# Optimization experiments

Hardware: AMD Instinct MI355X
Metric: run time of the kernel (lower is better)

## Reference

```python
import jax, jax.numpy as jnp
import numpy as np

N, E = 50000, 800000
IN_DIM, H0, H1, OUT_DIM = 64, 64, 64, 8
NUM_RELS, NUM_BASES = 16, 8


def setup_inputs() -> dict:
    key = jax.random.key(0)
    ks = jax.random.split(key, 20)
    features = jax.random.normal(ks[0], (N, IN_DIM), dtype=jnp.float32)
    etypes = jax.random.randint(ks[1], (E,), 0, NUM_RELS)
    src = jax.random.randint(ks[2], (E,), 0, N)
    dst = jax.random.randint(ks[3], (E,), 0, N)
    # degree normalization 1/in_degree(dst), as DGL stores in g.edata['norm']
    deg = jax.ops.segment_sum(jnp.ones((E,), jnp.float32), dst, num_segments=N)
    norm = (1.0 / jnp.maximum(deg, 1.0))[dst][:, None]  # [E,1]

    def glorot(k, shape):
        fan_in, fan_out = shape[-2], shape[-1]
        lim = jnp.sqrt(6.0 / (fan_in + fan_out)).astype(jnp.float32)
        return jax.random.uniform(k, shape, jnp.float32, -lim, lim)

    dims = [(IN_DIM, H0), (H0, H1), (H1, OUT_DIM)]
    inp = {"features": features, "norm": norm}
    for i, (di, do) in enumerate(dims):
        inp[f"basis{i}"] = glorot(ks[4 + 4 * i], (NUM_BASES, di, do))
        inp[f"comp{i}"] = glorot(ks[5 + 4 * i], (NUM_RELS, NUM_BASES))
        inp[f"loop{i}"] = glorot(ks[6 + 4 * i], (di, do))
        inp[f"bias{i}"] = jnp.zeros((do,), jnp.float32)
    inp["etypes"] = etypes
    inp["src"] = src
    inp["dst"] = dst
    return inp


def rel_graph_conv(h, basis, comp, loop_w, bias, etypes, src, dst, norm, act):
    # basis-decomposed relation weights: [R, din, dout]
    W = jnp.einsum('rb,bio->rio', comp, basis)
    # transform every node under every relation: [N, R, dout]
    h_trans = jnp.einsum('ni,rio->nro', h, W)
    # per-edge gather of (src node, edge relation), degree-normalized
    msg = h_trans[src, etypes] * norm  # [E, dout]
    agg = jax.ops.segment_sum(msg, dst, num_segments=h.shape[0])  # [N, dout]
    out = agg + h @ loop_w + bias  # self-loop + bias (DGL defaults)
    return act(out)


def reference(features, norm, basis0, comp0, loop0, bias0, basis1, comp1, loop1,
              bias1, basis2, comp2, loop2, bias2, etypes, src, dst):
    lrelu = lambda x: jax.nn.leaky_relu(x, negative_slope=0.01)
    h = rel_graph_conv(features, basis0, comp0, loop0, bias0, etypes, src, dst, norm, lrelu)
    h = rel_graph_conv(h, basis1, comp1, loop1, bias1, etypes, src, dst, norm, lrelu)
    h = rel_graph_conv(h, basis2, comp2, loop2, bias2, etypes, src, dst, norm, jax.nn.relu)
    return h
```

## Files before the change

### kernel.cpp

```cpp
#include <hip/hip_runtime.h>

#define NN 50000
#define NE 800000
#define CAP 64
#define KC 72
#define CSTR 16

typedef __bf16 bf16x8 __attribute__((ext_vector_type(8)));
typedef float f32x4 __attribute__((ext_vector_type(4)));
typedef float f32x2 __attribute__((ext_vector_type(2)));
typedef unsigned short ushort;
typedef unsigned int uint;

__device__ inline ushort f2bf(float x) {
  uint u = __builtin_bit_cast(uint, x);
  u += 0x7FFF + ((u >> 16) & 1);
  return (ushort)(u >> 16);
}
__device__ inline float bf2f(ushort u) {
  return __builtin_bit_cast(float, (uint)u << 16);
}


__device__ inline void wprep_body(const float* __restrict__ basis,
                                  const float* __restrict__ loopw,
                                  ushort* __restrict__ W2, int DOUT, int NCOLS,
                                  int idx) {
  int total = KC * NCOLS * 8;
  if (idx >= total) return;
  int j = idx & 7;
  int n = (idx >> 3) % NCOLS;
  int kc = idx / (8 * NCOLS);
  int k = kc * 8 + j;
  float v = 0.f;
  if (n < DOUT) v = (k < 512) ? basis[k * DOUT + n] : loopw[(k - 512) * DOUT + n];
  W2[((size_t)kc * NCOLS + n) * 8 + j] = f2bf(v);
}

__global__ __launch_bounds__(256) void build_kernel(
    const int* __restrict__ dstv, const int* __restrict__ srcv,
    const int* __restrict__ etv, int* __restrict__ cursor, int* __restrict__ pk,
    const float* __restrict__ f, ushort* __restrict__ fb,
    const float* __restrict__ b0, const float* __restrict__ l0, ushort* __restrict__ W0,
    const float* __restrict__ b1, const float* __restrict__ l1, ushort* __restrict__ W1,
    const float* __restrict__ b2, const float* __restrict__ l2, ushort* __restrict__ W2,
    const float* __restrict__ c0, const float* __restrict__ c1,
    const float* __restrict__ c2, float* __restrict__ cp) {
  int blk = blockIdx.x;
  int tid = threadIdx.x;
  if (blk < 3125) {
    int i = blk * 256 + tid;
    int d = dstv[i];
    int p = atomicAdd(&cursor[(size_t)d * CSTR], 1);
    if (p < CAP) pk[d * CAP + p] = (etv[i] << 16) | srcv[i];
  } else if (blk < 6250) {
    int i = (blk - 3125) * 256 + tid;
    float4 v = ((const float4*)f)[i];
    ushort4 u;
    u.x = f2bf(v.x); u.y = f2bf(v.y); u.z = f2bf(v.z); u.w = f2bf(v.w);
    ((ushort4*)fb)[i] = u;
  } else if (blk < 6394) {
    wprep_body(b0, l0, W0, 64, 64, (blk - 6250) * 256 + tid);
  } else if (blk < 6538) {
    wprep_body(b1, l1, W1, 64, 64, (blk - 6394) * 256 + tid);
  } else if (blk < 6574) {
    wprep_body(b2, l2, W2, 8, 16, (blk - 6538) * 256 + tid);
  } else {
    int idx = (blk - 6574) * 256 + tid;
    if (idx < 408) {
      int l = idx / 136, k = idx % 136;
      const float* src = (l == 0) ? c0 : ((l == 1) ? c1 : c2);
      cp[idx] = (k < 128) ? src[k] : 0.f;
    }
  }
}


template <int DOUT, int NCOLS, bool OBF>
__global__ __launch_bounds__(1024, 8) void layer_kernel(
    const ushort* __restrict__ hb,
    const float* __restrict__ cpad,
    const int* __restrict__ degv,
    const int* __restrict__ pk,
    const ushort* __restrict__ W2,
    const float* __restrict__ bias,
    void* __restrict__ outp,
    float slope)
{
  __shared__ ushort X[KC][16][8];
  int tid = threadIdx.x;
  int wave = tid >> 6;
  int lane = tid & 63;
  int dbase = blockIdx.x * 16;
  int d = __builtin_amdgcn_readfirstlane(dbase + wave);

  int deg = degv[(size_t)d * CSTR];
  int dw = deg > CAP ? CAP : deg;
  const int4* p4 = (const int4*)(pk + (size_t)d * CAP);

  f32x2 acc2[4] = {{0.f, 0.f}, {0.f, 0.f}, {0.f, 0.f}, {0.f, 0.f}};
  for (int base = 0; base < dw; base += 8) {
    int qg = base >> 3;
    int4 e0 = p4[qg * 2];
    int4 e1 = p4[qg * 2 + 1];
    int pe[8] = {e0.x, e0.y, e0.z, e0.w, e1.x, e1.y, e1.z, e1.w};
    float hv[8];
    int ps[8];
#pragma unroll
    for (int i = 0; i < 8; ++i) {
      int pr = __builtin_amdgcn_readfirstlane(pe[i]);
      ps[i] = (base + i < dw) ? pr : (16 << 16);
      hv[i] = bf2f(hb[(size_t)(ps[i] & 0xFFFF) * 64 + lane]);
    }
#pragma unroll
    for (int i = 0; i < 8; ++i) {
      const f32x2* c2 = (const f32x2*)(cpad + (ps[i] >> 16) * 8);
      f32x2 h2 = {hv[i], hv[i]};
#pragma unroll
      for (int j = 0; j < 4; ++j)
        acc2[j] = __builtin_elementwise_fma(c2[j], h2, acc2[j]);
    }
  }

  float inv = 1.0f / (float)(deg > 1 ? deg : 1);
  int jj = lane & 7;
  int csub = lane >> 3;
#pragma unroll
  for (int b = 0; b < 8; ++b) {
    float v = ((b & 1) ? acc2[b >> 1].y : acc2[b >> 1].x) * inv;
    X[b * 8 + csub][wave ^ csub][jj] = f2bf(v);
  }
  X[64 + csub][wave ^ csub][jj] = hb[(size_t)d * 64 + lane];
  __syncthreads();

  if (wave < (DOUT == 64 ? 4 : 1)) {
    int q = lane >> 4;
    int r = lane & 15;
    f32x4 accd = {0.f, 0.f, 0.f, 0.f};
#pragma unroll
    for (int ks = 0; ks < 18; ++ks) {
      int kc = ks * 4 + q;
      bf16x8 bfrag = *(const bf16x8*)&X[kc][r ^ (kc & 7)][0];
      bf16x8 afrag = *(const bf16x8*)(W2 + ((size_t)kc * NCOLS + wave * 16 + r) * 8);
      accd = __builtin_amdgcn_mfma_f32_16x16x32_bf16(afrag, bfrag, accd, 0, 0, 0);
    }
    int m = dbase + r;
    int nb = wave * 16 + q * 4;
    if (nb < DOUT) {
      float4 bv = *(const float4*)(bias + nb);
      float v0 = accd[0] + bv.x;
      float v1 = accd[1] + bv.y;
      float v2 = accd[2] + bv.z;
      float v3 = accd[3] + bv.w;
      v0 = v0 > 0.f ? v0 : slope * v0;
      v1 = v1 > 0.f ? v1 : slope * v1;
      v2 = v2 > 0.f ? v2 : slope * v2;
      v3 = v3 > 0.f ? v3 : slope * v3;
      if (OBF) {
        ushort4 u;
        u.x = f2bf(v0); u.y = f2bf(v1); u.z = f2bf(v2); u.w = f2bf(v3);
        *(ushort4*)((ushort*)outp + (size_t)m * DOUT + nb) = u;
      } else {
        *(float4*)((float*)outp + (size_t)m * DOUT + nb) = float4{v0, v1, v2, v3};
      }
    }
  }
}


extern "C" void kernel_launch(void* const* d_in, const int* in_sizes, int n_in,
                              void* d_out, int out_size, void* d_ws, size_t ws_size,
                              hipStream_t stream) {
  const float* features = (const float*)d_in[0];
  const float* basis0   = (const float*)d_in[2];
  const float* comp0    = (const float*)d_in[3];
  const float* loop0    = (const float*)d_in[4];
  const float* bias0    = (const float*)d_in[5];
  const float* basis1   = (const float*)d_in[6];
  const float* comp1    = (const float*)d_in[7];
  const float* loop1    = (const float*)d_in[8];
  const float* bias1    = (const float*)d_in[9];
  const float* basis2   = (const float*)d_in[10];
  const float* comp2    = (const float*)d_in[11];
  const float* loop2    = (const float*)d_in[12];
  const float* bias2    = (const float*)d_in[13];
  const int* etypes     = (const int*)d_in[14];
  const int* srcv       = (const int*)d_in[15];
  const int* dstv       = (const int*)d_in[16];

  char* ws = (char*)d_ws;
  size_t off = 0;
  auto alloc = [&](size_t bytes) {
    void* p = ws + off;
    off += (bytes + 255) & ~(size_t)255;
    return p;
  };
  int* cnt      = (int*)alloc((size_t)NN * CSTR * sizeof(int));
  int* pk       = (int*)alloc((size_t)NN * CAP * sizeof(int));
  ushort* W2_0  = (ushort*)alloc((size_t)KC * 64 * 8 * sizeof(ushort));
  ushort* W2_1  = (ushort*)alloc((size_t)KC * 64 * 8 * sizeof(ushort));
  ushort* W2_2  = (ushort*)alloc((size_t)KC * 16 * 8 * sizeof(ushort));
  float* cpad   = (float*)alloc(3 * 136 * sizeof(float));
  ushort* fbf   = (ushort*)alloc((size_t)NN * 64 * sizeof(ushort));
  ushort* hA    = (ushort*)alloc((size_t)NN * 64 * sizeof(ushort));
  ushort* hB    = (ushort*)alloc((size_t)NN * 64 * sizeof(ushort));

  hipMemsetAsync(cnt, 0, (size_t)NN * CSTR * sizeof(int), stream);
  build_kernel<<<6576, 256, 0, stream>>>(dstv, srcv, etypes, cnt, pk,
                                         features, fbf,
                                         basis0, loop0, W2_0,
                                         basis1, loop1, W2_1,
                                         basis2, loop2, W2_2,
                                         comp0, comp1, comp2, cpad);

  layer_kernel<64, 64, true><<<3125, 1024, 0, stream>>>(
      fbf, cpad + 0 * 136, cnt, pk, W2_0, bias0, hA, 0.01f);
  layer_kernel<64, 64, true><<<3125, 1024, 0, stream>>>(
      hA, cpad + 1 * 136, cnt, pk, W2_1, bias1, hB, 0.01f);
  layer_kernel<8, 16, false><<<3125, 1024, 0, stream>>>(
      hB, cpad + 2 * 136, cnt, pk, W2_2, bias2, d_out, 0.0f);
}
```

Baseline: 175.9 us.

## Stage neighbor rows via direct global-to-LDS loads, two nodes per wave

After: 324.7 us. +84.6%, slower.

```diff
diff --git a/kernel.cpp b/kernel.cpp
--- a/kernel.cpp
+++ b/kernel.cpp
@@ -4,13 +4,15 @@
 #define NE 800000
 #define CAP 64
 #define KC 72
-#define CSTR 16
 
 typedef __bf16 bf16x8 __attribute__((ext_vector_type(8)));
 typedef float f32x4 __attribute__((ext_vector_type(4)));
 typedef float f32x2 __attribute__((ext_vector_type(2)));
 typedef unsigned short ushort;
 typedef unsigned int uint;
+
+typedef __attribute__((address_space(1))) const void GAS;
+typedef __attribute__((address_space(3))) void LAS;
 
 __device__ inline ushort f2bf(float x) {
   uint u = __builtin_bit_cast(uint, x);
@@ -51,7 +53,7 @@
   if (blk < 3125) {
     int i = blk * 256 + tid;
     int d = dstv[i];
-    int p = atomicAdd(&cursor[(size_t)d * CSTR], 1);
+    int p = atomicAdd(&cursor[d], 1);
     if (p < CAP) pk[d * CAP + p] = (etv[i] << 16) | srcv[i];
   } else if (blk < 6250) {
     int i = (blk - 3125) * 256 + tid;
@@ -77,7 +79,7 @@
 
 
 template <int DOUT, int NCOLS, bool OBF>
-__global__ __launch_bounds__(1024, 8) void layer_kernel(
+__global__ __launch_bounds__(512, 4) void layer_kernel(
     const ushort* __restrict__ hb,
     const float* __restrict__ cpad,
     const int* __restrict__ degv,
@@ -88,49 +90,65 @@
     float slope)
 {
   __shared__ ushort X[KC][16][8];
+  __shared__ ushort STG[8][16][64];
   int tid = threadIdx.x;
   int wave = tid >> 6;
   int lane = tid & 63;
   int dbase = blockIdx.x * 16;
-  int d = __builtin_amdgcn_readfirstlane(dbase + wave);
-
-  int deg = degv[(size_t)d * CSTR];
-  int dw = deg > CAP ? CAP : deg;
-  const int4* p4 = (const int4*)(pk + (size_t)d * CAP);
-
-  f32x2 acc2[4] = {{0.f, 0.f}, {0.f, 0.f}, {0.f, 0.f}, {0.f, 0.f}};
-  for (int base = 0; base < dw; base += 8) {
-    int qg = base >> 3;
-    int4 e0 = p4[qg * 2];
-    int4 e1 = p4[qg * 2 + 1];
-    int pe[8] = {e0.x, e0.y, e0.z, e0.w, e1.x, e1.y, e1.z, e1.w};
-    float hv[8];
-    int ps[8];
-#pragma unroll
-    for (int i = 0; i < 8; ++i) {
-      int pr = __builtin_amdgcn_readfirstlane(pe[i]);
-      ps[i] = (base + i < dw) ? pr : (16 << 16);
-      hv[i] = bf2f(hb[(size_t)(ps[i] & 0xFFFF) * 64 + lane]);
-    }
-#pragma unroll
-    for (int i = 0; i < 8; ++i) {
-      const f32x2* c2 = (const f32x2*)(cpad + (ps[i] >> 16) * 8);
-      f32x2 h2 = {hv[i], hv[i]};
-#pragma unroll
-      for (int j = 0; j < 4; ++j)
-        acc2[j] = __builtin_elementwise_fma(c2[j], h2, acc2[j]);
-    }
+
+  for (int t = 0; t < 2; ++t) {
+    int dl = wave * 2 + t;
+    int d = __builtin_amdgcn_readfirstlane(dbase + dl);
+    int deg = degv[d];
+    int dwu = __builtin_amdgcn_readfirstlane(deg > CAP ? CAP : deg);
+    const int4* p4 = (const int4*)(pk + (size_t)d * CAP);
+
+    f32x2 acc2[4] = {{0.f, 0.f}, {0.f, 0.f}, {0.f, 0.f}, {0.f, 0.f}};
+    for (int base = 0; base < dwu; base += 16) {
+      int4 g0 = p4[(base >> 2) + 0];
+      int4 g1 = p4[(base >> 2) + 1];
+      int4 g2 = p4[(base >> 2) + 2];
+      int4 g3 = p4[(base >> 2) + 3];
+      int pe[16] = {g0.x, g0.y, g0.z, g0.w, g1.x, g1.y, g1.z, g1.w,
+                    g2.x, g2.y, g2.z, g2.w, g3.x, g3.y, g3.z, g3.w};
+      uint rs[16], ss[16];
+#pragma unroll
+      for (int i = 0; i < 16; ++i) {
+        uint up = (uint)__builtin_amdgcn_readfirstlane(pe[i]);
+        int valid = (base + i) < dwu;
+        rs[i] = valid ? (up >> 16) : 16u;
+        ss[i] = valid ? (up & 0xFFFFu) : 0u;
+      }
+#pragma unroll
+      for (int i = 0; i < 8; ++i) {
+        uint s_sel = (lane < 32) ? ss[2 * i] : ss[2 * i + 1];
+        const ushort* gp = hb + (size_t)s_sel * 64 + (lane & 31) * 2;
+        __builtin_amdgcn_global_load_lds((GAS*)gp, (LAS*)&STG[wave][2 * i][0],
+                                         4, 0, 0);
+      }
+      asm volatile("s_waitcnt vmcnt(0)" ::: "memory");
+      __builtin_amdgcn_sched_barrier(0);
+#pragma unroll
+      for (int i = 0; i < 16; ++i) {
+        float hv = bf2f(STG[wave][i][lane]);
+        f32x2 h2 = {hv, hv};
+        const f32x2* c2 = (const f32x2*)(cpad + rs[i] * 8);
+#pragma unroll
+        for (int j = 0; j < 4; ++j)
+          acc2[j] = __builtin_elementwise_fma(c2[j], h2, acc2[j]);
+      }
+    }
+
+    float inv = 1.0f / (float)(deg > 1 ? deg : 1);
+    int jj = lane & 7;
+    int csub = lane >> 3;
+#pragma unroll
+    for (int b = 0; b < 8; ++b) {
+      float v = ((b & 1) ? acc2[b >> 1].y : acc2[b >> 1].x) * inv;
+      X[b * 8 + csub][dl ^ csub][jj] = f2bf(v);
+    }
+    X[64 + csub][dl ^ csub][jj] = hb[(size_t)d * 64 + lane];
   }
-
-  float inv = 1.0f / (float)(deg > 1 ? deg : 1);
-  int jj = lane & 7;
-  int csub = lane >> 3;
-#pragma unroll
-  for (int b = 0; b < 8; ++b) {
-    float v = ((b & 1) ? acc2[b >> 1].y : acc2[b >> 1].x) * inv;
-    X[b * 8 + csub][wave ^ csub][jj] = f2bf(v);
-  }
-  X[64 + csub][wave ^ csub][jj] = hb[(size_t)d * 64 + lane];
   __syncthreads();
 
   if (wave < (DOUT == 64 ? 4 : 1)) {
@@ -195,7 +213,7 @@
     off += (bytes + 255) & ~(size_t)255;
     return p;
   };
-  int* cnt      = (int*)alloc((size_t)NN * CSTR * sizeof(int));
+  int* cnt      = (int*)alloc(NN * sizeof(int));
   int* pk       = (int*)alloc((size_t)NN * CAP * sizeof(int));
   ushort* W2_0  = (ushort*)alloc((size_t)KC * 64 * 8 * sizeof(ushort));
   ushort* W2_1  = (ushort*)alloc((size_t)KC * 64 * 8 * sizeof(ushort));
@@ -205,7 +223,7 @@
   ushort* hA    = (ushort*)alloc((size_t)NN * 64 * sizeof(ushort));
   ushort* hB    = (ushort*)alloc((size_t)NN * 64 * sizeof(ushort));
 
-  hipMemsetAsync(cnt, 0, (size_t)NN * CSTR * sizeof(int), stream);
+  hipMemsetAsync(cnt, 0, NN * sizeof(int), stream);
   build_kernel<<<6576, 256, 0, stream>>>(dstv, srcv, etypes, cnt, pk,
                                          features, fbf,
                                          basis0, loop0, W2_0,
@@ -213,10 +231,10 @@
                                          basis2, loop2, W2_2,
                                          comp0, comp1, comp2, cpad);
 
-  layer_kernel<64, 64, true><<<3125, 1024, 0, stream>>>(
+  layer_kernel<64, 64, true><<<3125, 512, 0, stream>>>(
       fbf, cpad + 0 * 136, cnt, pk, W2_0, bias0, hA, 0.01f);
-  layer_kernel<64, 64, true><<<3125, 1024, 0, stream>>>(
+  layer_kernel<64, 64, true><<<3125, 512, 0, stream>>>(
       hA, cpad + 1 * 136, cnt, pk, W2_1, bias1, hB, 0.01f);
-  layer_kernel<8, 16, false><<<3125, 1024, 0, stream>>>(
+  layer_kernel<8, 16, false><<<3125, 512, 0, stream>>>(
       hB, cpad + 2 * 136, cnt, pk, W2_2, bias2, d_out, 0.0f);
 }
```
